# Kernel optimization log

Measured on AMD Instinct MI355X. Metric: run time of the kernel, lower is better.

Reference implementation:

```python
import jax, jax.numpy as jnp
import numpy as np

N, E, U, L = 10000, 320000, 256, 3


def setup_inputs() -> dict:
    key = jax.random.key(0)
    ks = jax.random.split(key, 16)
    s = 0.05
    p = {}
    p["pos"] = jax.random.normal(ks[0], (N, 2), jnp.float32)
    p["edge_attr_in"] = jax.random.uniform(ks[1], (E, 1), jnp.float32)
    p["edge_index"] = jax.random.randint(ks[2], (2, E), 0, N)
    p["Wp"] = jax.random.normal(ks[3], (2, U), jnp.float32) * s
    p["bp"] = jnp.zeros((U,), jnp.float32)
    p["Wa"] = jax.random.normal(ks[4], (1, U), jnp.float32) * s
    p["ba"] = jnp.zeros((U,), jnp.float32)
    p["W1"] = jax.random.normal(ks[5], (L, U, U), jnp.float32) * s
    p["b1"] = jnp.zeros((L, U), jnp.float32)
    p["W2"] = jax.random.normal(ks[6], (L, U, U), jnp.float32) * s
    p["b2"] = jnp.zeros((L, U), jnp.float32)
    p["We"] = jax.random.normal(ks[7], (L + 1, U, U), jnp.float32) * s
    p["be"] = jnp.zeros((L + 1, U), jnp.float32)
    p["Ws"] = jax.random.normal(ks[8], (L + 1, U, U), jnp.float32) * s
    p["Wt"] = jax.random.normal(ks[9], (L + 1, U, U), jnp.float32) * s
    p["Wm1"] = jax.random.normal(ks[10], (U + 1, U // 2), jnp.float32) * s
    p["bm1"] = jnp.zeros((U // 2,), jnp.float32)
    p["alpha"] = 0.25 * jnp.ones((1,), jnp.float32)  # PReLU default slope
    p["Wm2"] = jax.random.normal(ks[11], (U // 2, 1), jnp.float32) * s
    p["bm2"] = jnp.zeros((1,), jnp.float32)
    return p


def _forward(pos, edge_attr_in, edge_index, Wp, bp, Wa, ba, W1, b1, W2, b2,
             We, be, Ws, Wt, Wm1, bm1, alpha, Wm2, bm2):
    src, dst = edge_index[0], edge_index[1]
    x = pos @ Wp + bp                      # [N, U]
    e = edge_attr_in @ Wa + ba             # [E, U]

    def edge_update(x, e, l):
        # ResEdgeLinear: residual edge update from endpoint nodes + edge feats
        return e + jax.nn.relu(e @ We[l] + x[src] @ Ws[l] + x[dst] @ Wt[l] + be[l])

    for l in range(L):
        # ResNodeConv: gated gather-linear-scatter with residual
        gate = jax.nn.sigmoid(e)                                   # [E, U]
        msg = gate * (x[src] @ W2[l] + b2[l])                      # [E, U]
        agg = jax.ops.segment_sum(msg, dst, num_segments=N)        # [N, U]
        x_new = x + jax.nn.relu(x @ W1[l] + b1[l] + agg)
        e_new = edge_update(x, e, l)  # simultaneous update: both use old (x, e)
        x, e = x_new, e_new
    e = edge_update(x, e, L)

    h = jnp.concatenate([e, edge_attr_in[:, :1]], axis=-1) @ Wm1 + bm1
    h = jnp.where(h > 0, h, alpha * h)  # PReLU
    return h @ Wm2 + bm2                # [E, 1] logits


def reference(pos, edge_attr_in, edge_index, Wp, bp, Wa, ba, W1, b1, W2, b2,
              We, be, Ws, Wt, Wm1, bm1, alpha, Wm2, bm2):
    return _forward(pos, edge_attr_in, edge_index, Wp, bp, Wa, ba, W1, b1,
                    W2, b2, We, be, Ws, Wt, Wm1, bm1, alpha, Wm2, bm2)
```

## Files before the change

### kernel.cpp

```cpp
#include <hip/hip_runtime.h>
#include <stdint.h>

#define N_NODES 10000
#define N_EDGES 320000

using bf16x8 = __attribute__((ext_vector_type(8))) short;
using fp32x4 = __attribute__((ext_vector_type(4))) float;
using u16x8 = __attribute__((ext_vector_type(8))) unsigned short;
using i32x4 = __attribute__((ext_vector_type(4))) int;

__device__ __forceinline__ float bf2f(unsigned short u) {
  union { unsigned int i; float f; } v; v.i = ((unsigned int)u) << 16; return v.f;
}
__device__ __forceinline__ unsigned short f2bf(float f) {
  union { float f; unsigned int i; } v; v.f = f;
  unsigned int x = v.i;
  x += 0x7fffu + ((x >> 16) & 1u);
  return (unsigned short)(x >> 16);
}

#define A_POS 0
#define A_EA 20000
#define A_WP 340000
#define A_BP 340512
#define A_WA 340768
#define A_BA 341024
#define A_W1 341280
#define A_B1 537888
#define A_W2 538656
#define A_B2 735264
#define A_WE 736032
#define A_BE 998176
#define A_WS 999200
#define A_WT 1261344
#define A_WM1 1523488
#define A_BM1 1556384
#define A_AL 1556512
#define A_WM2 1556544
#define A_BM2 1556672
#define ARENA_USED 1556673
#define ARENA_TOT 1556736

__constant__ int g_off[19] = {A_POS, A_EA, A_WP, A_BP, A_WA, A_BA, A_W1, A_B1,
                              A_W2, A_B2, A_WE, A_BE, A_WS, A_WT, A_WM1,
                              A_BM1, A_AL, A_WM2, A_BM2};

struct Ptrs { const void* p[19]; };

__global__ void k_detect(const unsigned short* wpraw, int* flag) {
  __shared__ int cnt;
  int tid = threadIdx.x;
  if (tid == 0) cnt = 0;
  __syncthreads();
  float v0 = bf2f(wpraw[tid]);
  float v1 = bf2f(wpraw[256 + tid]);
  int big = (fabsf(v0) > 100.f ? 1 : 0) + (fabsf(v1) > 100.f ? 1 : 0);
  atomicAdd(&cnt, big);
  __syncthreads();
  if (tid == 0) *flag = (cnt > 10) ? 1 : 0;
}

__global__ void k_cast(Ptrs ptrs, const int* __restrict__ flag,
                       unsigned short* __restrict__ arena) {
  int a = blockIdx.x * 256 + threadIdx.x;
  if (a >= ARENA_USED) return;
  int z = 0;
#pragma unroll
  for (int j = 1; j < 19; ++j) if (a >= g_off[j]) z = j;
  int i = a - g_off[z];
  float v;
  if (*flag) v = ((const float*)ptrs.p[z])[i];
  else       v = bf2f(((const unsigned short*)ptrs.p[z])[i]);
  arena[a] = f2bf(v);
}

__global__ void k_prep(const unsigned short* __restrict__ arena,
                       unsigned short* nodeBT, unsigned short* WeT,
                       unsigned short* Wm1T, unsigned short* biascat) {
  int z = blockIdx.z;
  int i = blockIdx.x * 256 + threadIdx.x;
  if (z == 19) {
    if (i < 3072) {
      int l = i >> 10, j = i & 1023;
      unsigned short v = 0;
      if (j < 256) v = arena[A_B1 + l * 256 + j];
      else if (j < 512) v = arena[A_B2 + l * 256 + (j - 256)];
      biascat[i] = v;
    } else if (i < 3584) {
      biascat[i] = 0;
    }
    return;
  }
  const unsigned short* src; unsigned short* dst; int srcN = 256;
  if (z < 3)       {                 src = arena + A_W1 + z * 65536; dst = nodeBT + z * 262144; }
  else if (z < 6)  { int l = z - 3;  src = arena + A_W2 + l * 65536; dst = nodeBT + l * 262144 + 65536; }
  else if (z < 10) { int l = z - 6;  src = arena + A_WS + l * 65536;
                     dst = (l < 3) ? nodeBT + l * 262144 + 131072 : nodeBT + 786432; }
  else if (z < 14) { int l = z - 10; src = arena + A_WT + l * 65536;
                     dst = (l < 3) ? nodeBT + l * 262144 + 196608 : nodeBT + 786432 + 65536; }
  else if (z < 18) { int l = z - 14; src = arena + A_WE + l * 65536; dst = WeT + l * 65536; }
  else             { src = arena + A_WM1; dst = Wm1T; srcN = 128; }
  if (i < srcN * 256) {
    int k = i & 255, n = i >> 8;
    dst[i] = src[k * srcN + n];
  }
}

__global__ void k_init_x(const unsigned short* __restrict__ arena,
                         float* __restrict__ xf, unsigned short* __restrict__ xbf) {
  int n = blockIdx.x, c = threadIdx.x;
  float p0 = bf2f(arena[A_POS + 2 * n]), p1 = bf2f(arena[A_POS + 2 * n + 1]);
  float v = fmaf(p0, bf2f(arena[A_WP + c]),
                 fmaf(p1, bf2f(arena[A_WP + 256 + c]), bf2f(arena[A_BP + c])));
  long idx = ((long)n << 8) + c;
  xf[idx] = v;
  xbf[idx] = f2bf(v);
}

__global__ void k_hist(const int* __restrict__ dstA, int* __restrict__ deg) {
  int i = blockIdx.x * 256 + threadIdx.x;
  if (i < N_EDGES) {
    int d = dstA[i];
    if ((unsigned)d < N_NODES) atomicAdd(&deg[d], 1);
  }
}

__global__ void k_scan(const int* __restrict__ deg, int* __restrict__ rowptr,
                       int* __restrict__ cursor) {
  __shared__ int part[256];
  int tid = threadIdx.x;
  int base = tid * 40;
  int s = 0;
  for (int i = 0; i < 40; ++i) {
    int idx = base + i;
    if (idx < N_NODES) s += deg[idx];
  }
  part[tid] = s;
  __syncthreads();
  if (tid == 0) {
    int run = 0;
    for (int i = 0; i < 256; ++i) { int t = part[i]; part[i] = run; run += t; }
    rowptr[N_NODES] = run;
  }
  __syncthreads();
  int run = part[tid];
  for (int i = 0; i < 40; ++i) {
    int idx = base + i;
    if (idx < N_NODES) { rowptr[idx] = run; cursor[idx] = run; run += deg[idx]; }
  }
}

__global__ void k_fill(const int* __restrict__ dstA, const int* __restrict__ srcA,
                       const unsigned short* __restrict__ arena,
                       int* __restrict__ cursor, int* __restrict__ eid,
                       int* __restrict__ csrc, int* __restrict__ cdst,
                       unsigned short* __restrict__ eaC) {
  int i = blockIdx.x * 256 + threadIdx.x;
  if (i < N_EDGES) {
    int d = dstA[i]; if ((unsigned)d >= N_NODES) d = 0;
    int p = atomicAdd(&cursor[d], 1);
    if ((unsigned)p < N_EDGES) {
      eid[p] = i;
      int s = srcA[i]; if ((unsigned)s >= N_NODES) s = 0;
      csrc[p] = s;
      cdst[p] = d;
      eaC[p] = arena[A_EA + i];
    }
  }
}

#define SM_PITCH 528

template <bool NT, int ROWS>
__device__ __forceinline__ void stage_tile(char* smc, const unsigned short* src,
                                           long rowBase) {
  int tid = threadIdx.x;
#pragma unroll
  for (int it = 0; it < ROWS / 8; ++it) {
    int lin = it * 256 + tid;
    int row = lin >> 5, g = lin & 31;
    const i32x4* p = (const i32x4*)((const char*)src + ((rowBase + row) << 9) + (g << 4));
    i32x4 v = NT ? __builtin_nontemporal_load(p) : *p;
    *(i32x4*)(smc + row * SM_PITCH + (g << 4)) = v;
  }
}

template <int MT, int NTT>
__device__ __forceinline__ void gemm_swap(const char* smc, const unsigned short* WT,
                                          int colBase, fp32x4 (&acc)[MT][NTT]) {
  const int lane = threadIdx.x & 63;
  const int q = lane >> 4, ll = lane & 15;
  const int llperm = ((ll >> 2) * (MT * 4)) + (ll & 3);
#pragma unroll
  for (int ks = 0; ks < 8; ++ks) {
    bf16x8 a[MT];
#pragma unroll
    for (int mt = 0; mt < MT; ++mt) {
      int oc = colBase + llperm + mt * 4;
      a[mt] = *(const bf16x8*)((const char*)WT + ((long)oc << 9) + (ks << 6) + (q << 4));
    }
    bf16x8 b[NTT];
#pragma unroll
    for (int nt = 0; nt < NTT; ++nt)
      b[nt] = *(const bf16x8*)(smc + (nt * 16 + ll) * SM_PITCH + (ks << 6) + (q << 4));
#pragma unroll
    for (int mt = 0; mt < MT; ++mt)
#pragma unroll
      for (int nt = 0; nt < NTT; ++nt)
        acc[mt][nt] = __builtin_amdgcn_mfma_f32_16x16x32_bf16(a[mt], b[nt], acc[mt][nt], 0, 0, 0);
  }
}

template <int NTT>
__device__ __forceinline__ void edge_epilogue(
    char* smc, const fp32x4 (&acc)[4][NTT], const int* s_src, const int* s_dst,
    const unsigned short* XW, int xw_pitch, int xs_off, int xt_off,
    const unsigned short* bePtr, int cb, int ll) {
  u16x8 be0 = *(const u16x8*)(bePtr + cb);
  u16x8 be1 = *(const u16x8*)(bePtr + cb + 8);
#pragma unroll
  for (int nt = 0; nt < NTT; ++nt) {
    int el = nt * 16 + ll;
    int sn = s_src[el], dn = s_dst[el];
    const unsigned short* xsrow = XW + (long)sn * xw_pitch + xs_off + cb;
    const unsigned short* xtrow = XW + (long)dn * xw_pitch + xt_off + cb;
    u16x8 xs0 = *(const u16x8*)(xsrow);
    u16x8 xs1 = *(const u16x8*)(xsrow + 8);
    u16x8 xt0 = *(const u16x8*)(xtrow);
    u16x8 xt1 = *(const u16x8*)(xtrow + 8);
    u16x8* slot = (u16x8*)(smc + el * SM_PITCH + cb * 2);
    u16x8 er0 = slot[0], er1 = slot[1];
    u16x8 o0, o1;
#pragma unroll
    for (int mt = 0; mt < 4; ++mt)
#pragma unroll
      for (int r = 0; r < 4; ++r) {
        int i = mt * 4 + r;
        float xsv = bf2f(i < 8 ? xs0[i] : xs1[i - 8]);
        float xtv = bf2f(i < 8 ? xt0[i] : xt1[i - 8]);
        float erv = bf2f(i < 8 ? er0[i] : er1[i - 8]);
        float bev = bf2f(i < 8 ? be0[i] : be1[i - 8]);
        float v = acc[mt][nt][r] + xsv + xtv + bev;
        v = fmaxf(v, 0.f);
        unsigned short ob = f2bf(erv + v);
        if (i < 8) o0[i] = ob; else o1[i - 8] = ob;
      }
    slot[0] = o0;
    slot[1] = o1;
  }
}

template <int MODE>
__global__ __launch_bounds__(256, 2) void k_edge(
    unsigned short* __restrict__ e, const unsigned short* __restrict__ WT,
    const unsigned short* __restrict__ XW, int xw_pitch, int xs_off, int xt_off,
    const unsigned short* __restrict__ bePtr, const unsigned short* __restrict__ arena,
    const unsigned short* __restrict__ eaC,
    const int* __restrict__ csrc, const int* __restrict__ cdst) {
  __shared__ int4 sm4[128 * 33];
  __shared__ int s_src[128];
  __shared__ int s_dst[128];
  char* smc = (char*)sm4;
  const long tileBase = (long)blockIdx.x * 128;
  const int tid = threadIdx.x;
  const int wave = tid >> 6, lane = tid & 63;
  const int q = lane >> 4, ll = lane & 15;
  const int colBase = wave * 64;

  if (MODE == 0) {
#pragma unroll
    for (int it = 0; it < 16; ++it) {
      int lin = it * 256 + tid;
      int row = lin >> 5, g = lin & 31;
      float eav = bf2f(eaC[tileBase + row]);
      int c0 = g * 8;
      bf16x8 ov;
#pragma unroll
      for (int j = 0; j < 8; ++j) {
        float f = fmaf(eav, bf2f(arena[A_WA + c0 + j]), bf2f(arena[A_BA + c0 + j]));
        ((unsigned short*)&ov)[j] = f2bf(f);
      }
      *(bf16x8*)(smc + row * SM_PITCH + (g << 4)) = ov;
    }
  } else {
    stage_tile<true, 128>(smc, e, tileBase);
  }
  if (tid < 128) {
    long edge = tileBase + tid;
    int s = csrc[edge]; if ((unsigned)s >= N_NODES) s = 0;
    int d = cdst[edge]; if ((unsigned)d >= N_NODES) d = 0;
    s_src[tid] = s;
    s_dst[tid] = d;
  }
  __syncthreads();

  fp32x4 acc[4][8];
#pragma unroll
  for (int mt = 0; mt < 4; ++mt)
#pragma unroll
    for (int nt = 0; nt < 8; ++nt) acc[mt][nt] = 0.f;
  gemm_swap<4, 8>(smc, WT, colBase, acc);
  __syncthreads();

  edge_epilogue<8>(smc, acc, s_src, s_dst, XW, xw_pitch, xs_off, xt_off,
                   bePtr, colBase + q * 16, ll);
  __syncthreads();

#pragma unroll
  for (int it = 0; it < 16; ++it) {
    int lin = it * 256 + tid;
    int row = lin >> 5, g = lin & 31;
    i32x4 v = *(const i32x4*)(smc + row * SM_PITCH + (g << 4));
    __builtin_nontemporal_store(v, (i32x4*)((char*)e + ((tileBase + row) << 9) + (g << 4)));
  }
}

__global__ __launch_bounds__(256, 2) void k_edge_last2(
    const unsigned short* __restrict__ e, const unsigned short* __restrict__ WeT2,
    const unsigned short* __restrict__ WeT3,
    const unsigned short* __restrict__ XW2, const unsigned short* __restrict__ XW3,
    const unsigned short* __restrict__ arena, const unsigned short* __restrict__ eaC,
    const int* __restrict__ csrc, const int* __restrict__ cdst,
    const unsigned short* __restrict__ Wm1T, const int* __restrict__ eid,
    const int* __restrict__ flag, void* __restrict__ out) {
  __shared__ int4 sm4[128 * 33];
  __shared__ int s_src[128];
  __shared__ int s_dst[128];
  char* smc = (char*)sm4;
  const long tileBase = (long)blockIdx.x * 128;
  const int tid = threadIdx.x;
  const int wave = tid >> 6, lane = tid & 63;
  const int q = lane >> 4, ll = lane & 15;
  const int colBase = wave * 64;

  stage_tile<true, 128>(smc, e, tileBase);
  if (tid < 128) {
    long edge = tileBase + tid;
    int s = csrc[edge]; if ((unsigned)s >= N_NODES) s = 0;
    int d = cdst[edge]; if ((unsigned)d >= N_NODES) d = 0;
    s_src[tid] = s;
    s_dst[tid] = d;
  }
  __syncthreads();

  fp32x4 acc[4][8];
#pragma unroll
  for (int mt = 0; mt < 4; ++mt)
#pragma unroll
    for (int nt = 0; nt < 8; ++nt) acc[mt][nt] = 0.f;
  gemm_swap<4, 8>(smc, WeT2, colBase, acc);
  __syncthreads();
  edge_epilogue<8>(smc, acc, s_src, s_dst, XW2, 1024, 512, 768,
                   arena + A_BE + 2 * 256, colBase + q * 16, ll);
  __syncthreads();

#pragma unroll
  for (int mt = 0; mt < 4; ++mt)
#pragma unroll
    for (int nt = 0; nt < 8; ++nt) acc[mt][nt] = 0.f;
  gemm_swap<4, 8>(smc, WeT3, colBase, acc);
  __syncthreads();
  edge_epilogue<8>(smc, acc, s_src, s_dst, XW3, 512, 0, 256,
                   arena + A_BE + 3 * 256, colBase + q * 16, ll);
  __syncthreads();

  fp32x4 acc2[2][8];
#pragma unroll
  for (int mt = 0; mt < 2; ++mt)
#pragma unroll
    for (int nt = 0; nt < 8; ++nt) acc2[mt][nt] = 0.f;
  const int colBase2 = wave * 32;
  gemm_swap<2, 8>(smc, Wm1T, colBase2, acc2);

  const int cb2 = colBase2 + q * 8;
  float alphaf = bf2f(arena[A_AL]);
  float bmc[8], wl[8], w2c[8];
#pragma unroll
  for (int i = 0; i < 8; ++i) {
    bmc[i] = bf2f(arena[A_BM1 + cb2 + i]);
    wl[i] = bf2f(arena[A_WM1 + 32768 + cb2 + i]);
    w2c[i] = bf2f(arena[A_WM2 + cb2 + i]);
  }
  __syncthreads();
  float* part = (float*)smc;
#pragma unroll
  for (int nt = 0; nt < 8; ++nt) {
    int el = nt * 16 + ll;
    float eav = bf2f(eaC[tileBase + el]);
    float ps = 0.f;
#pragma unroll
    for (int mt = 0; mt < 2; ++mt)
#pragma unroll
      for (int r = 0; r < 4; ++r) {
        int i = mt * 4 + r;
        float h = acc2[mt][nt][r] + bmc[i] + eav * wl[i];
        h = (h > 0.f) ? h : alphaf * h;
        ps += h * w2c[i];
      }
    ps += __shfl_xor(ps, 16, 64);
    ps += __shfl_xor(ps, 32, 64);
    if (q == 0) part[el * 4 + wave] = ps;
  }
  __syncthreads();
  if (tid < 128) {
    float t = part[tid * 4] + part[tid * 4 + 1] + part[tid * 4 + 2] + part[tid * 4 + 3]
            + bf2f(arena[A_BM2]);
    long row = tileBase + tid;
    int oe = eid[row]; if ((unsigned)oe >= N_EDGES) oe = 0;
    if (*flag) ((float*)out)[oe] = t;
    else       ((unsigned short*)out)[oe] = f2bf(t);
  }
}

__global__ __launch_bounds__(256, 2) void k_node_gemm(
    const unsigned short* __restrict__ xbf, const unsigned short* __restrict__ WT,
    const unsigned short* __restrict__ bias, unsigned short* __restrict__ out,
    int out_pitch) {
  __shared__ int4 sm4[128 * 33];
  char* smc = (char*)sm4;
  const long tileBase = (long)blockIdx.x * 128;
  {
    int tid = threadIdx.x;
#pragma unroll
    for (int it = 0; it < 16; ++it) {
      int lin = it * 256 + tid;
      int row = lin >> 5, g = lin & 31;
      long rg = tileBase + row;
      if (rg > N_NODES - 1) rg = N_NODES - 1;
      i32x4 v = *(const i32x4*)((const char*)xbf + (rg << 9) + (g << 4));
      *(i32x4*)(smc + row * SM_PITCH + (g << 4)) = v;
    }
  }
  __syncthreads();
  fp32x4 acc[2][8];
#pragma unroll
  for (int mt = 0; mt < 2; ++mt)
#pragma unroll
    for (int nt = 0; nt < 8; ++nt) acc[mt][nt] = 0.f;
  const int tid = threadIdx.x, wave = tid >> 6, lane = tid & 63;
  const int q = lane >> 4, ll = lane & 15;
  const int colBase = blockIdx.y * 128 + wave * 32;
  gemm_swap<2, 8>(smc, WT, colBase, acc);

  const int cb = colBase + q * 8;
  u16x8 bs8 = *(const u16x8*)(bias + cb);

#pragma unroll
  for (int nt = 0; nt < 8; ++nt) {
    long nn = tileBase + nt * 16 + ll;
    if (nn >= N_NODES) continue;
    u16x8 o0;
#pragma unroll
    for (int mt = 0; mt < 2; ++mt)
#pragma unroll
      for (int r = 0; r < 4; ++r) {
        int i = mt * 4 + r;
        o0[i] = f2bf(acc[mt][nt][r] + bf2f(bs8[i]));
      }
    *(u16x8*)(out + nn * out_pitch + cb) = o0;
  }
}

template <bool FIRST>
__global__ void k_agg(const int* __restrict__ csrc, const int* __restrict__ cdst,
                      const unsigned short* __restrict__ e,
                      const unsigned short* __restrict__ eaC,
                      const unsigned short* __restrict__ arena,
                      const unsigned short* __restrict__ XW, int xw_pitch, int x2_off,
                      float* __restrict__ agg) {
  __shared__ int s_src[64];
  __shared__ int s_dst[64];
  const long base = (long)blockIdx.x * 64;
  const int c = threadIdx.x;
  if (c < 64) {
    long r = base + c;
    int s = csrc[r]; if ((unsigned)s >= N_NODES) s = 0;
    int d = cdst[r]; if ((unsigned)d >= N_NODES) d = 0;
    s_src[c] = s;
    s_dst[c] = d;
  }
  __syncthreads();
  float wac = 0.f, bac = 0.f;
  if (FIRST) { wac = bf2f(arena[A_WA + c]); bac = bf2f(arena[A_BA + c]); }
  float a = 0.f;
  int run = s_dst[0];
  for (int b8 = 0; b8 < 64; b8 += 8) {
    float evv[8], x2v[8];
#pragma unroll
    for (int j = 0; j < 8; ++j) {
      int row = b8 + j;
      if (FIRST) evv[j] = fmaf(bf2f(eaC[base + row]), wac, bac);
      else evv[j] = bf2f(__builtin_nontemporal_load(e + ((base + row) << 8) + c));
      x2v[j] = bf2f(XW[(long)s_src[row] * xw_pitch + x2_off + c]);
    }
#pragma unroll
    for (int j = 0; j < 8; ++j) {
      int d = s_dst[b8 + j];
      if (d != run) {
        atomicAdd(&agg[((long)run << 8) + c], a);
        a = 0.f;
        run = d;
      }
      float gate = 1.f / (1.f + __expf(-evv[j]));
      a = fmaf(gate, x2v[j], a);
    }
  }
  atomicAdd(&agg[((long)run << 8) + c], a);
}

__global__ void k_node_update(float* __restrict__ xf, unsigned short* __restrict__ xbf,
                              const unsigned short* __restrict__ XW,
                              float* __restrict__ agg) {
  int n = blockIdx.x, c = threadIdx.x;
  long idx = ((long)n << 8) + c;
  float av = agg[idx];
  agg[idx] = 0.f;
  float t = bf2f(XW[((long)n << 10) + c]) + av;
  float nx = xf[idx] + fmaxf(t, 0.f);
  xf[idx] = nx;
  xbf[idx] = f2bf(nx);
}

extern "C" void kernel_launch(void* const* d_in, const int* in_sizes, int n_in,
                              void* d_out, int out_size, void* d_ws, size_t ws_size,
                              hipStream_t stream) {
  const int* eidx = (const int*)d_in[2];
  const int* srcA = eidx;
  const int* dstA = eidx + N_EDGES;
  (void)in_sizes; (void)n_in; (void)out_size;

  char* ws = (char*)d_ws;
  size_t off = 0;
  auto alloc = [&](size_t bytes) -> char* {
    char* p = ws + off;
    off = (off + bytes + 255) & ~(size_t)255;
    return p;
  };
  unsigned short* e_buf   = (unsigned short*)alloc((size_t)N_EDGES * 256 * 2);
  float*          xf      = (float*)alloc((size_t)N_NODES * 256 * 4);
  unsigned short* xbf     = (unsigned short*)alloc((size_t)N_NODES * 256 * 2);
  unsigned short* XW      = (unsigned short*)alloc((size_t)N_NODES * 1024 * 2);
  unsigned short* XW3     = (unsigned short*)alloc((size_t)N_NODES * 512 * 2);
  float*          agg     = (float*)alloc((size_t)N_NODES * 256 * 4);
  unsigned short* nodeBT  = (unsigned short*)alloc((size_t)917504 * 2);
  unsigned short* WeT     = (unsigned short*)alloc((size_t)4 * 65536 * 2);
  unsigned short* Wm1T    = (unsigned short*)alloc((size_t)32768 * 2);
  unsigned short* biascat = (unsigned short*)alloc((size_t)3584 * 2);
  unsigned short* arena   = (unsigned short*)alloc((size_t)ARENA_TOT * 2);
  int* deg    = (int*)alloc((size_t)N_NODES * 4);
  int* rowptr = (int*)alloc((size_t)(N_NODES + 1) * 4);
  int* cursor = (int*)alloc((size_t)N_NODES * 4);
  int* eid    = (int*)alloc((size_t)N_EDGES * 4);
  int* csrc   = (int*)alloc((size_t)N_EDGES * 4);
  int* cdst   = (int*)alloc((size_t)N_EDGES * 4);
  unsigned short* eaC = (unsigned short*)alloc((size_t)N_EDGES * 2);
  int* flag   = (int*)alloc(4);
  if (ws_size < off) return;

  Ptrs ptrs;
  {
    int map[19] = {0, 1, 3, 4, 5, 6, 7, 8, 9, 10, 11, 12, 13, 14, 15, 16, 17, 18, 19};
    for (int j = 0; j < 19; ++j) ptrs.p[j] = d_in[map[j]];
  }

  dim3 blk(256);
  k_detect<<<dim3(1), blk, 0, stream>>>((const unsigned short*)d_in[3], flag);
  k_cast<<<dim3((ARENA_USED + 255) / 256), blk, 0, stream>>>(ptrs, flag, arena);
  k_prep<<<dim3(256, 1, 20), blk, 0, stream>>>(arena, nodeBT, WeT, Wm1T, biascat);
  k_init_x<<<dim3(N_NODES), blk, 0, stream>>>(arena, xf, xbf);
  hipMemsetAsync(deg, 0, (size_t)N_NODES * 4, stream);
  hipMemsetAsync(agg, 0, (size_t)N_NODES * 256 * 4, stream);
  k_hist<<<dim3(N_EDGES / 256), blk, 0, stream>>>(dstA, deg);
  k_scan<<<dim3(1), blk, 0, stream>>>(deg, rowptr, cursor);
  k_fill<<<dim3(N_EDGES / 256), blk, 0, stream>>>(dstA, srcA, arena, cursor, eid, csrc,
                                                  cdst, eaC);

  for (int l = 0; l < 3; ++l) {
    k_node_gemm<<<dim3(79, 8), blk, 0, stream>>>(xbf, nodeBT + l * 262144,
                                                 biascat + l * 1024, XW, 1024);
    if (l == 0)
      k_agg<true><<<dim3(N_EDGES / 64), blk, 0, stream>>>(csrc, cdst, e_buf, eaC, arena,
                                                          XW, 1024, 256, agg);
    else
      k_agg<false><<<dim3(N_EDGES / 64), blk, 0, stream>>>(csrc, cdst, e_buf, eaC, arena,
                                                           XW, 1024, 256, agg);
    if (l == 0)
      k_edge<0><<<dim3(N_EDGES / 128), blk, 0, stream>>>(
          e_buf, WeT, XW, 1024, 512, 768, arena + A_BE, arena, eaC, csrc, cdst);
    else if (l == 1)
      k_edge<1><<<dim3(N_EDGES / 128), blk, 0, stream>>>(
          e_buf, WeT + l * 65536, XW, 1024, 512, 768, arena + A_BE + l * 256,
          arena, eaC, csrc, cdst);
    k_node_update<<<dim3(N_NODES), blk, 0, stream>>>(xf, xbf, XW, agg);
  }
  k_node_gemm<<<dim3(79, 4), blk, 0, stream>>>(xbf, nodeBT + 786432, biascat + 3072, XW3, 512);
  k_edge_last2<<<dim3(N_EDGES / 128), blk, 0, stream>>>(
      e_buf, WeT + 2 * 65536, WeT + 3 * 65536, XW, XW3, arena, eaC,
      csrc, cdst, Wm1T, eid, flag, d_out);
}
```

Measured before the change: 886.0 us.

## Fuse next-layer node GEMM into edge kernel and fold memsets into init kernels

Reorders the layer loop so the node update runs before the edge update. The next layer's node GEMM is then co-launched as extra blocks inside the edge-update kernel, with ping-pong XW buffers so the edge blocks read the old projections while the node blocks write new ones. This removes separate node-GEMM launches and lets the small node GEMM fill idle CUs during the large edge kernel. The two memsets are also folded into k_detect and k_init_x to cut launches. The cost is an extra XW buffer and a heterogeneous kernel whose register and LDS use is sized for the heavier edge path.

```diff
diff --git a/kernel.cpp b/kernel.cpp
--- a/kernel.cpp
+++ b/kernel.cpp
@@ -47,17 +47,21 @@
 
 struct Ptrs { const void* p[19]; };
 
-__global__ void k_detect(const unsigned short* wpraw, int* flag) {
-  __shared__ int cnt;
-  int tid = threadIdx.x;
-  if (tid == 0) cnt = 0;
-  __syncthreads();
-  float v0 = bf2f(wpraw[tid]);
-  float v1 = bf2f(wpraw[256 + tid]);
-  int big = (fabsf(v0) > 100.f ? 1 : 0) + (fabsf(v1) > 100.f ? 1 : 0);
-  atomicAdd(&cnt, big);
-  __syncthreads();
-  if (tid == 0) *flag = (cnt > 10) ? 1 : 0;
+__global__ void k_detect(const unsigned short* wpraw, int* flag, int* deg) {
+  int i = blockIdx.x * 256 + threadIdx.x;
+  if (i < N_NODES) deg[i] = 0;
+  if (blockIdx.x == 0) {
+    __shared__ int cnt;
+    int tid = threadIdx.x;
+    if (tid == 0) cnt = 0;
+    __syncthreads();
+    float v0 = bf2f(wpraw[tid]);
+    float v1 = bf2f(wpraw[256 + tid]);
+    int big = (fabsf(v0) > 100.f ? 1 : 0) + (fabsf(v1) > 100.f ? 1 : 0);
+    atomicAdd(&cnt, big);
+    __syncthreads();
+    if (tid == 0) *flag = (cnt > 10) ? 1 : 0;
+  }
 }
 
 __global__ void k_cast(Ptrs ptrs, const int* __restrict__ flag,
@@ -107,7 +111,8 @@
 }
 
 __global__ void k_init_x(const unsigned short* __restrict__ arena,
-                         float* __restrict__ xf, unsigned short* __restrict__ xbf) {
+                         float* __restrict__ xf, unsigned short* __restrict__ xbf,
+                         float* __restrict__ agg) {
   int n = blockIdx.x, c = threadIdx.x;
   float p0 = bf2f(arena[A_POS + 2 * n]), p1 = bf2f(arena[A_POS + 2 * n + 1]);
   float v = fmaf(p0, bf2f(arena[A_WP + c]),
@@ -115,6 +120,7 @@
   long idx = ((long)n << 8) + c;
   xf[idx] = v;
   xbf[idx] = f2bf(v);
+  agg[idx] = 0.f;
 }
 
 __global__ void k_hist(const int* __restrict__ dstA, int* __restrict__ deg) {
@@ -170,6 +176,7 @@
 }
 
 #define SM_PITCH 528
+#define EDGE_BLOCKS (N_EDGES / 128)
 
 template <bool NT, int ROWS>
 __device__ __forceinline__ void stage_tile(char* smc, const unsigned short* src,
@@ -251,67 +258,109 @@
 }
 
 template <int MODE>
-__global__ __launch_bounds__(256, 2) void k_edge(
-    unsigned short* __restrict__ e, const unsigned short* __restrict__ WT,
-    const unsigned short* __restrict__ XW, int xw_pitch, int xs_off, int xt_off,
+__global__ __launch_bounds__(256, 2) void k_fat(
+    unsigned short* __restrict__ e, const unsigned short* __restrict__ WT_edge,
+    const unsigned short* __restrict__ XW_edge,
     const unsigned short* __restrict__ bePtr, const unsigned short* __restrict__ arena,
     const unsigned short* __restrict__ eaC,
-    const int* __restrict__ csrc, const int* __restrict__ cdst) {
+    const int* __restrict__ csrc, const int* __restrict__ cdst,
+    const unsigned short* __restrict__ xbf, const unsigned short* __restrict__ WT_node,
+    const unsigned short* __restrict__ bias, unsigned short* __restrict__ XW_out) {
   __shared__ int4 sm4[128 * 33];
   __shared__ int s_src[128];
   __shared__ int s_dst[128];
   char* smc = (char*)sm4;
-  const long tileBase = (long)blockIdx.x * 128;
   const int tid = threadIdx.x;
   const int wave = tid >> 6, lane = tid & 63;
   const int q = lane >> 4, ll = lane & 15;
-  const int colBase = wave * 64;
-
-  if (MODE == 0) {
+
+  if (blockIdx.x < EDGE_BLOCKS) {
+    const long tileBase = (long)blockIdx.x * 128;
+    const int colBase = wave * 64;
+    if (MODE == 0) {
+#pragma unroll
+      for (int it = 0; it < 16; ++it) {
+        int lin = it * 256 + tid;
+        int row = lin >> 5, g = lin & 31;
+        float eav = bf2f(eaC[tileBase + row]);
+        int c0 = g * 8;
+        bf16x8 ov;
+#pragma unroll
+        for (int j = 0; j < 8; ++j) {
+          float f = fmaf(eav, bf2f(arena[A_WA + c0 + j]), bf2f(arena[A_BA + c0 + j]));
+          ((unsigned short*)&ov)[j] = f2bf(f);
+        }
+        *(bf16x8*)(smc + row * SM_PITCH + (g << 4)) = ov;
+      }
+    } else {
+      stage_tile<true, 128>(smc, e, tileBase);
+    }
+    if (tid < 128) {
+      long edge = tileBase + tid;
+      int s = csrc[edge]; if ((unsigned)s >= N_NODES) s = 0;
+      int d = cdst[edge]; if ((unsigned)d >= N_NODES) d = 0;
+      s_src[tid] = s;
+      s_dst[tid] = d;
+    }
+    __syncthreads();
+
+    fp32x4 acc[4][8];
+#pragma unroll
+    for (int mt = 0; mt < 4; ++mt)
+#pragma unroll
+      for (int nt = 0; nt < 8; ++nt) acc[mt][nt] = 0.f;
+    gemm_swap<4, 8>(smc, WT_edge, colBase, acc);
+    __syncthreads();
+
+    edge_epilogue<8>(smc, acc, s_src, s_dst, XW_edge, 1024, 512, 768,
+                     bePtr, colBase + q * 16, ll);
+    __syncthreads();
+
 #pragma unroll
     for (int it = 0; it < 16; ++it) {
       int lin = it * 256 + tid;
       int row = lin >> 5, g = lin & 31;
-      float eav = bf2f(eaC[tileBase + row]);
-      int c0 = g * 8;
-      bf16x8 ov;
-#pragma unroll
-      for (int j = 0; j < 8; ++j) {
-        float f = fmaf(eav, bf2f(arena[A_WA + c0 + j]), bf2f(arena[A_BA + c0 + j]));
-        ((unsigned short*)&ov)[j] = f2bf(f);
-      }
-      *(bf16x8*)(smc + row * SM_PITCH + (g << 4)) = ov;
+      i32x4 v = *(const i32x4*)(smc + row * SM_PITCH + (g << 4));
+      __builtin_nontemporal_store(v, (i32x4*)((char*)e + ((tileBase + row) << 9) + (g << 4)));
     }
   } else {
-    stage_tile<true, 128>(smc, e, tileBase);
-  }
-  if (tid < 128) {
-    long edge = tileBase + tid;
-    int s = csrc[edge]; if ((unsigned)s >= N_NODES) s = 0;
-    int d = cdst[edge]; if ((unsigned)d >= N_NODES) d = 0;
-    s_src[tid] = s;
-    s_dst[tid] = d;
-  }
-  __syncthreads();
-
-  fp32x4 acc[4][8];
-#pragma unroll
-  for (int mt = 0; mt < 4; ++mt)
-#pragma unroll
-    for (int nt = 0; nt < 8; ++nt) acc[mt][nt] = 0.f;
-  gemm_swap<4, 8>(smc, WT, colBase, acc);
-  __syncthreads();
-
-  edge_epilogue<8>(smc, acc, s_src, s_dst, XW, xw_pitch, xs_off, xt_off,
-                   bePtr, colBase + q * 16, ll);
-  __syncthreads();
-
-#pragma unroll
-  for (int it = 0; it < 16; ++it) {
-    int lin = it * 256 + tid;
-    int row = lin >> 5, g = lin & 31;
-    i32x4 v = *(const i32x4*)(smc + row * SM_PITCH + (g << 4));
-    __builtin_nontemporal_store(v, (i32x4*)((char*)e + ((tileBase + row) << 9) + (g << 4)));
+    int b = blockIdx.x - EDGE_BLOCKS;
+    int bx = b % 79, by = b / 79;
+    const long tileBase = (long)bx * 128;
+#pragma unroll
+    for (int it = 0; it < 16; ++it) {
+      int lin = it * 256 + tid;
+      int row = lin >> 5, g = lin & 31;
+      long rg = tileBase + row;
+      if (rg > N_NODES - 1) rg = N_NODES - 1;
+      i32x4 v = *(const i32x4*)((const char*)xbf + (rg << 9) + (g << 4));
+      *(i32x4*)(smc + row * SM_PITCH + (g << 4)) = v;
+    }
+    __syncthreads();
+    fp32x4 acc[2][8];
+#pragma unroll
+    for (int mt = 0; mt < 2; ++mt)
+#pragma unroll
+      for (int nt = 0; nt < 8; ++nt) acc[mt][nt] = 0.f;
+    const int colBase = by * 128 + wave * 32;
+    gemm_swap<2, 8>(smc, WT_node, colBase, acc);
+
+    const int cb = colBase + q * 8;
+    u16x8 bs8 = *(const u16x8*)(bias + cb);
+#pragma unroll
+    for (int nt = 0; nt < 8; ++nt) {
+      long nn = tileBase + nt * 16 + ll;
+      if (nn >= N_NODES) continue;
+      u16x8 o0;
+#pragma unroll
+      for (int mt = 0; mt < 2; ++mt)
+#pragma unroll
+        for (int r = 0; r < 4; ++r) {
+          int i = mt * 4 + r;
+          o0[i] = f2bf(acc[mt][nt][r] + bf2f(bs8[i]));
+        }
+      *(u16x8*)(XW_out + nn * 1024 + cb) = o0;
+    }
   }
 }
 
@@ -444,7 +493,6 @@
 
   const int cb = colBase + q * 8;
   u16x8 bs8 = *(const u16x8*)(bias + cb);
-
 #pragma unroll
   for (int nt = 0; nt < 8; ++nt) {
     long nn = tileBase + nt * 16 + ll;
@@ -539,7 +587,8 @@
   unsigned short* e_buf   = (unsigned short*)alloc((size_t)N_EDGES * 256 * 2);
   float*          xf      = (float*)alloc((size_t)N_NODES * 256 * 4);
   unsigned short* xbf     = (unsigned short*)alloc((size_t)N_NODES * 256 * 2);
-  unsigned short* XW      = (unsigned short*)alloc((size_t)N_NODES * 1024 * 2);
+  unsigned short* XWa     = (unsigned short*)alloc((size_t)N_NODES * 1024 * 2);
+  unsigned short* XWb     = (unsigned short*)alloc((size_t)N_NODES * 1024 * 2);
   unsigned short* XW3     = (unsigned short*)alloc((size_t)N_NODES * 512 * 2);
   float*          agg     = (float*)alloc((size_t)N_NODES * 256 * 4);
   unsigned short* nodeBT  = (unsigned short*)alloc((size_t)917504 * 2);
@@ -564,37 +613,33 @@
   }
 
   dim3 blk(256);
-  k_detect<<<dim3(1), blk, 0, stream>>>((const unsigned short*)d_in[3], flag);
+  k_detect<<<dim3(40), blk, 0, stream>>>((const unsigned short*)d_in[3], flag, deg);
   k_cast<<<dim3((ARENA_USED + 255) / 256), blk, 0, stream>>>(ptrs, flag, arena);
   k_prep<<<dim3(256, 1, 20), blk, 0, stream>>>(arena, nodeBT, WeT, Wm1T, biascat);
-  k_init_x<<<dim3(N_NODES), blk, 0, stream>>>(arena, xf, xbf);
-  hipMemsetAsync(deg, 0, (size_t)N_NODES * 4, stream);
-  hipMemsetAsync(agg, 0, (size_t)N_NODES * 256 * 4, stream);
+  k_init_x<<<dim3(N_NODES), blk, 0, stream>>>(arena, xf, xbf, agg);
   k_hist<<<dim3(N_EDGES / 256), blk, 0, stream>>>(dstA, deg);
   k_scan<<<dim3(1), blk, 0, stream>>>(deg, rowptr, cursor);
   k_fill<<<dim3(N_EDGES / 256), blk, 0, stream>>>(dstA, srcA, arena, cursor, eid, csrc,
                                                   cdst, eaC);
 
-  for (int l = 0; l < 3; ++l) {
-    k_node_gemm<<<dim3(79, 8), blk, 0, stream>>>(xbf, nodeBT + l * 262144,
-                                                 biascat + l * 1024, XW, 1024);
-    if (l == 0)
-      k_agg<true><<<dim3(N_EDGES / 64), blk, 0, stream>>>(csrc, cdst, e_buf, eaC, arena,
-                                                          XW, 1024, 256, agg);
-    else
-      k_agg<false><<<dim3(N_EDGES / 64), blk, 0, stream>>>(csrc, cdst, e_buf, eaC, arena,
-                                                           XW, 1024, 256, agg);
-    if (l == 0)
-      k_edge<0><<<dim3(N_EDGES / 128), blk, 0, stream>>>(
-          e_buf, WeT, XW, 1024, 512, 768, arena + A_BE, arena, eaC, csrc, cdst);
-    else if (l == 1)
-      k_edge<1><<<dim3(N_EDGES / 128), blk, 0, stream>>>(
-          e_buf, WeT + l * 65536, XW, 1024, 512, 768, arena + A_BE + l * 256,
-          arena, eaC, csrc, cdst);
-    k_node_update<<<dim3(N_NODES), blk, 0, stream>>>(xf, xbf, XW, agg);
-  }
+  k_node_gemm<<<dim3(79, 8), blk, 0, stream>>>(xbf, nodeBT, biascat, XWa, 1024);
+  k_agg<true><<<dim3(N_EDGES / 64), blk, 0, stream>>>(csrc, cdst, e_buf, eaC, arena,
+                                                      XWa, 1024, 256, agg);
+  k_node_update<<<dim3(N_NODES), blk, 0, stream>>>(xf, xbf, XWa, agg);
+  k_fat<0><<<dim3(EDGE_BLOCKS + 632), blk, 0, stream>>>(
+      e_buf, WeT, XWa, arena + A_BE, arena, eaC, csrc, cdst,
+      xbf, nodeBT + 262144, biascat + 1024, XWb);
+  k_agg<false><<<dim3(N_EDGES / 64), blk, 0, stream>>>(csrc, cdst, e_buf, eaC, arena,
+                                                       XWb, 1024, 256, agg);
+  k_node_update<<<dim3(N_NODES), blk, 0, stream>>>(xf, xbf, XWb, agg);
+  k_fat<1><<<dim3(EDGE_BLOCKS + 632), blk, 0, stream>>>(
+      e_buf, WeT + 65536, XWb, arena + A_BE + 256, arena, eaC, csrc, cdst,
+      xbf, nodeBT + 2 * 262144, biascat + 2048, XWa);
+  k_agg<false><<<dim3(N_EDGES / 64), blk, 0, stream>>>(csrc, cdst, e_buf, eaC, arena,
+                                                       XWa, 1024, 256, agg);
+  k_node_update<<<dim3(N_NODES), blk, 0, stream>>>(xf, xbf, XWa, agg);
   k_node_gemm<<<dim3(79, 4), blk, 0, stream>>>(xbf, nodeBT + 786432, biascat + 3072, XW3, 512);
-  k_edge_last2<<<dim3(N_EDGES / 128), blk, 0, stream>>>(
-      e_buf, WeT + 2 * 65536, WeT + 3 * 65536, XW, XW3, arena, eaC,
+  k_edge_last2<<<dim3(EDGE_BLOCKS), blk, 0, stream>>>(
+      e_buf, WeT + 2 * 65536, WeT + 3 * 65536, XWa, XW3, arena, eaC,
       csrc, cdst, Wm1T, eid, flag, d_out);
 }
```

Result: no change. 868.7 us (-1.9%).
